# Kernel optimization log

Hardware: AMD Instinct MI355X
Metric: run time of the kernel (lower is better)

## Reference

```python
import jax, jax.numpy as jnp
import numpy as np

N_NODES = 50000
N_EDGES = 800000
FEAT = 128


def setup_inputs() -> dict:
    key = jax.random.key(0)
    k1, k2, k3, k4 = jax.random.split(key, 4)
    x = jax.random.normal(k1, (N_NODES, FEAT), dtype=jnp.float32)
    a = jax.random.normal(k2, (FEAT, 1), dtype=jnp.float32) * (1.414 / np.sqrt(FEAT))
    row = jax.random.randint(k3, (N_EDGES,), 0, N_NODES, dtype=jnp.int64)
    col = jax.random.randint(k4, (N_EDGES,), 0, N_NODES, dtype=jnp.int64)
    return {"x": x, "a": a, "row": row, "col": col}


def reference(x, a, row, col):
    n = x.shape[0]
    # per-node score e = x @ a, squeezed to [N]
    e = jnp.squeeze(x @ a, axis=-1)
    # gather per-edge score from the destination (column) node, as in e[col]
    vals = e[col]                                            # [E]
    # sparse row-wise softmax (numerically stable via segment max)
    m = jax.ops.segment_max(vals, row, num_segments=n)       # [N]
    m = jnp.where(jnp.isfinite(m), m, 0.0)                   # empty rows -> 0
    ex = jnp.exp(vals - m[row])                              # [E]
    denom = jax.ops.segment_sum(ex, row, num_segments=n)     # [N]
    att = ex / denom[row]                                    # [E]
    # sparse-dense matmul: h[i] = sum_j att_ij * x[j]
    h_prime = jax.ops.segment_sum(att[:, None] * x[col], row, num_segments=n)
    return h_prime
```

## Files before the change

kernel.cpp:

```cpp
#include <hip/hip_runtime.h>
#include <hip/hip_bf16.h>
#include <math.h>

#define FEAT 128

__device__ __forceinline__ int pack_bf162(float lo, float hi) {
    __hip_bfloat162 b = __float22bfloat162_rn(make_float2(lo, hi));
    union { __hip_bfloat162 b; int i; } u;
    u.b = b;
    return u.i;
}

__device__ __forceinline__ float2 bf2_to_f2(int b) {
    union { int i; __hip_bfloat162 b; } u;
    u.i = b;
    return __bfloat1622float2(u.b);
}

__global__ void dot_hist_kernel(const float* __restrict__ x, const float* __restrict__ a,
                                const int* __restrict__ row,
                                float* __restrict__ exw, unsigned* __restrict__ cnt,
                                unsigned short* __restrict__ rank,
                                int2* __restrict__ xh, int n, int nE) {
    int tid = blockIdx.x * blockDim.x + threadIdx.x;
    if (tid < nE) {
        unsigned old = atomicAdd(&cnt[row[tid]], 1u);
        rank[tid] = (unsigned short)old;
    }
    int node = tid >> 5;
    int l = tid & 31;
    if (node >= n) return;
    float4 xv = ((const float4*)(x + (size_t)node * FEAT))[l];
    float4 av = ((const float4*)a)[l];
    int2 pk;
    pk.x = pack_bf162(xv.x, xv.y);
    pk.y = pack_bf162(xv.z, xv.w);
    xh[(size_t)node * 32 + l] = pk;
    float p = xv.x * av.x + xv.y * av.y + xv.z * av.z + xv.w * av.w;
    #pragma unroll
    for (int off = 16; off > 0; off >>= 1) p += __shfl_xor(p, off);
    if (l == 0) exw[node] = __expf(p);
}

__global__ void scan_kernel(const unsigned* __restrict__ cnt, int* __restrict__ rowptr,
                            unsigned* flags, int n, int nb) {
    __shared__ int sm[256];
    __shared__ int sprefix;
    int b = blockIdx.x;
    int i0 = (b << 10) + (int)threadIdx.x * 4;
    int v0 = (i0 + 0 < n) ? (int)cnt[i0 + 0] : 0;
    int v1 = (i0 + 1 < n) ? (int)cnt[i0 + 1] : 0;
    int v2 = (i0 + 2 < n) ? (int)cnt[i0 + 2] : 0;
    int v3 = (i0 + 3 < n) ? (int)cnt[i0 + 3] : 0;
    int t4 = v0 + v1 + v2 + v3;
    sm[threadIdx.x] = t4;
    __syncthreads();
    #pragma unroll
    for (int off = 1; off < 256; off <<= 1) {
        int u = (threadIdx.x >= (unsigned)off) ? sm[threadIdx.x - off] : 0;
        __syncthreads();
        sm[threadIdx.x] += u;
        __syncthreads();
    }
    if (threadIdx.x == 0)
        __hip_atomic_store(&flags[b], (unsigned)sm[255] + 1u, __ATOMIC_RELEASE,
                           __HIP_MEMORY_SCOPE_AGENT);
    if (threadIdx.x < 64) {
        int lane = threadIdx.x;
        unsigned pred = 0;
        if (lane < b) {
            unsigned f;
            do {
                f = __hip_atomic_load(&flags[lane], __ATOMIC_ACQUIRE,
                                      __HIP_MEMORY_SCOPE_AGENT);
            } while (f == 0u);
            pred = f - 1u;
        }
        #pragma unroll
        for (int off = 32; off > 0; off >>= 1) pred += __shfl_xor(pred, off);
        if (lane == 0) sprefix = (int)pred;
    }
    __syncthreads();
    int base = sprefix + sm[threadIdx.x] - t4;
    if (i0 + 0 < n) rowptr[i0 + 0] = base;
    if (i0 + 1 < n) rowptr[i0 + 1] = base + v0;
    if (i0 + 2 < n) rowptr[i0 + 2] = base + v0 + v1;
    if (i0 + 3 < n) rowptr[i0 + 3] = base + v0 + v1 + v2;
    if (b == nb - 1 && threadIdx.x == 255) rowptr[n] = sprefix + sm[255];
}

__global__ void fill_kernel(const int* __restrict__ row, const int* __restrict__ col,
                            const unsigned short* __restrict__ rank,
                            const int* __restrict__ rowptr,
                            unsigned short* __restrict__ ecol, int nE) {
    int k = (blockIdx.x * blockDim.x + threadIdx.x) * 4;
    if (k + 3 < nE) {
        int4 r4 = *(const int4*)(row + k);
        int4 c4 = *(const int4*)(col + k);
        uint2 rk = *(const uint2*)(rank + k);
        ecol[rowptr[r4.x] + (int)(rk.x & 0xFFFFu)] = (unsigned short)c4.x;
        ecol[rowptr[r4.y] + (int)(rk.x >> 16)]     = (unsigned short)c4.y;
        ecol[rowptr[r4.z] + (int)(rk.y & 0xFFFFu)] = (unsigned short)c4.z;
        ecol[rowptr[r4.w] + (int)(rk.y >> 16)]     = (unsigned short)c4.w;
    } else {
        for (; k < nE; ++k)
            ecol[rowptr[row[k]] + (int)rank[k]] = (unsigned short)col[k];
    }
}

__global__ void gather_kernel(const int2* __restrict__ xh,
                              const float* __restrict__ exw,
                              const int* __restrict__ rowptr,
                              const unsigned short* __restrict__ ecol,
                              float* __restrict__ h, int n) {
    __shared__ __align__(16) int2 sbuf[8][32];
    int g = threadIdx.x >> 5;
    int lane = threadIdx.x & 31;
    int node = (int)((blockIdx.x * blockDim.x + threadIdx.x) >> 5);
    if (node >= n) return;
    int s = rowptr[node];
    int eend = rowptr[node + 1];
    float4 acc = make_float4(0.f, 0.f, 0.f, 0.f);
    float wsum = 0.0f;
    const int4* sb4 = (const int4*)&sbuf[g][0];
    for (int base = s; base < eend; base += 32) {
        int idx = base + lane;
        float w = 0.0f;
        if (idx < eend) {
            int c = (int)ecol[idx];
            w = exw[c];
            sbuf[g][lane] = make_int2(c << 5, __float_as_int(w));
        }
        #pragma unroll
        for (int off = 16; off > 0; off >>= 1) w += __shfl_xor(w, off);
        wsum += w;
        int m = min(32, eend - base);
        int j = 0;
        for (; j + 4 <= m; j += 4) {
            int4 q0 = sb4[(j >> 1) + 0];
            int4 q1 = sb4[(j >> 1) + 1];
            int2 e0 = xh[q0.x + lane];
            int2 e1 = xh[q0.z + lane];
            int2 e2 = xh[q1.x + lane];
            int2 e3 = xh[q1.z + lane];
            float w0 = __int_as_float(q0.y), w1 = __int_as_float(q0.w);
            float w2 = __int_as_float(q1.y), w3 = __int_as_float(q1.w);
            float2 a0 = bf2_to_f2(e0.x), b0 = bf2_to_f2(e0.y);
            float2 a1 = bf2_to_f2(e1.x), b1 = bf2_to_f2(e1.y);
            float2 a2 = bf2_to_f2(e2.x), b2 = bf2_to_f2(e2.y);
            float2 a3 = bf2_to_f2(e3.x), b3 = bf2_to_f2(e3.y);
            acc.x += w0 * a0.x; acc.y += w0 * a0.y; acc.z += w0 * b0.x; acc.w += w0 * b0.y;
            acc.x += w1 * a1.x; acc.y += w1 * a1.y; acc.z += w1 * b1.x; acc.w += w1 * b1.y;
            acc.x += w2 * a2.x; acc.y += w2 * a2.y; acc.z += w2 * b2.x; acc.w += w2 * b2.y;
            acc.x += w3 * a3.x; acc.y += w3 * a3.y; acc.z += w3 * b3.x; acc.w += w3 * b3.y;
        }
        for (; j < m; ++j) {
            int2 p = sbuf[g][j];
            int2 e = xh[p.x + lane];
            float wj = __int_as_float(p.y);
            float2 aa = bf2_to_f2(e.x), bb = bf2_to_f2(e.y);
            acc.x += wj * aa.x; acc.y += wj * aa.y;
            acc.z += wj * bb.x; acc.w += wj * bb.y;
        }
    }
    float inv = (eend > s) ? 1.0f / wsum : 0.0f;
    float4 out;
    out.x = acc.x * inv;
    out.y = acc.y * inv;
    out.z = acc.z * inv;
    out.w = acc.w * inv;
    ((float4*)(h + (size_t)node * FEAT))[lane] = out;
}

extern "C" void kernel_launch(void* const* d_in, const int* in_sizes, int n_in,
                              void* d_out, int out_size, void* d_ws, size_t ws_size,
                              hipStream_t stream) {
    const float* x = (const float*)d_in[0];
    const float* a = (const float*)d_in[1];
    const int* row = (const int*)d_in[2];
    const int* col = (const int*)d_in[3];
    int n  = in_sizes[0] / FEAT;
    int nE = in_sizes[2];
    float* h = (float*)d_out;
    int nb = (n + 1023) / 1024;

    char* p = (char*)d_ws;
    auto alloc = [&](size_t bytes) { char* q = p; p += (bytes + 15) & ~(size_t)15; return q; };
    unsigned* cnt        = (unsigned*)alloc((size_t)n * 4);
    unsigned* flags      = (unsigned*)alloc(64 * 4);
    float* exw           = (float*)alloc((size_t)n * 4);
    int* rowptr          = (int*)alloc((size_t)(n + 1) * 4);
    unsigned short* rank = (unsigned short*)alloc((size_t)nE * 2);
    unsigned short* ecol = (unsigned short*)alloc((size_t)nE * 2);
    int2* xh             = (int2*)alloc((size_t)n * 32 * 8);

    hipMemsetAsync(cnt, 0, ((size_t)n + 64) * sizeof(unsigned), stream);

    int t1 = (n * 32 > nE) ? n * 32 : nE;
    dot_hist_kernel<<<(t1 + 255) / 256, 256, 0, stream>>>(x, a, row, exw, cnt, rank,
                                                          xh, n, nE);
    scan_kernel<<<nb, 256, 0, stream>>>(cnt, rowptr, flags, n, nb);
    fill_kernel<<<(nE / 4 + 255) / 256, 256, 0, stream>>>(row, col, rank, rowptr,
                                                          ecol, nE);
    gather_kernel<<<(n * 32 + 255) / 256, 256, 0, stream>>>(xh, exw, rowptr, ecol, h, n);
}
```

Baseline: 166.9 us.

## Fuse all stages into one persistent kernel with software grid barriers

Replaces the four separate launches (histogram/dot, scan, fill, gather) with one persistent kernel of 1440 blocks that runs the stages in sequence, separated by atomic-counter grid barriers. The gather stage also changes from 32 lanes with 8-byte loads per node to 16 lanes with 16-byte loads, so each group covers more features per lane. The aim is to remove launch gaps and tail effects between kernels. In exchange it relies on all 1440 blocks being co-resident (launch bounds 6 blocks per CU), with deadlock risk if they are not, and it adds barrier spin cost.

After: 575.2 us. 3.45x slower.

```diff
diff --git a/kernel.cpp b/kernel.cpp
--- a/kernel.cpp
+++ b/kernel.cpp
@@ -3,6 +3,9 @@
 #include <math.h>
 
 #define FEAT 128
+#define GRID 1440
+#define TPB  256
+#define GSZ  (GRID * TPB)
 
 __device__ __forceinline__ int pack_bf162(float lo, float hi) {
     __hip_bfloat162 b = __float22bfloat162_rn(make_float2(lo, hi));
@@ -17,159 +20,186 @@
     return __bfloat1622float2(u.b);
 }
 
-__global__ void dot_hist_kernel(const float* __restrict__ x, const float* __restrict__ a,
-                                const int* __restrict__ row,
-                                float* __restrict__ exw, unsigned* __restrict__ cnt,
-                                unsigned short* __restrict__ rank,
-                                int2* __restrict__ xh, int n, int nE) {
-    int tid = blockIdx.x * blockDim.x + threadIdx.x;
-    if (tid < nE) {
-        unsigned old = atomicAdd(&cnt[row[tid]], 1u);
-        rank[tid] = (unsigned short)old;
-    }
-    int node = tid >> 5;
-    int l = tid & 31;
-    if (node >= n) return;
-    float4 xv = ((const float4*)(x + (size_t)node * FEAT))[l];
-    float4 av = ((const float4*)a)[l];
-    int2 pk;
-    pk.x = pack_bf162(xv.x, xv.y);
-    pk.y = pack_bf162(xv.z, xv.w);
-    xh[(size_t)node * 32 + l] = pk;
-    float p = xv.x * av.x + xv.y * av.y + xv.z * av.z + xv.w * av.w;
-    #pragma unroll
-    for (int off = 16; off > 0; off >>= 1) p += __shfl_xor(p, off);
-    if (l == 0) exw[node] = __expf(p);
-}
-
-__global__ void scan_kernel(const unsigned* __restrict__ cnt, int* __restrict__ rowptr,
-                            unsigned* flags, int n, int nb) {
+__device__ __forceinline__ void fma8(float* acc, int4 v, float w) {
+    float2 f0 = bf2_to_f2(v.x), f1 = bf2_to_f2(v.y);
+    float2 f2 = bf2_to_f2(v.z), f3 = bf2_to_f2(v.w);
+    acc[0] += w * f0.x; acc[1] += w * f0.y;
+    acc[2] += w * f1.x; acc[3] += w * f1.y;
+    acc[4] += w * f2.x; acc[5] += w * f2.y;
+    acc[6] += w * f3.x; acc[7] += w * f3.y;
+}
+
+__device__ __forceinline__ void gridbar(unsigned* bsync, unsigned target) {
+    __syncthreads();
+    if (threadIdx.x == 0) {
+        __hip_atomic_fetch_add(bsync, 1u, __ATOMIC_ACQ_REL, __HIP_MEMORY_SCOPE_AGENT);
+        unsigned v = __hip_atomic_load(bsync, __ATOMIC_ACQUIRE, __HIP_MEMORY_SCOPE_AGENT);
+        while (v < target) {
+            __builtin_amdgcn_s_sleep(2);
+            v = __hip_atomic_load(bsync, __ATOMIC_ACQUIRE, __HIP_MEMORY_SCOPE_AGENT);
+        }
+    }
+    __syncthreads();
+}
+
+extern "C" __global__ void __launch_bounds__(TPB, 6)
+gat_fused(const float* __restrict__ x, const float* __restrict__ a,
+          const int* __restrict__ row, const int* __restrict__ col,
+          float* __restrict__ h,
+          unsigned* __restrict__ cnt, unsigned* __restrict__ flags,
+          unsigned* __restrict__ bsync,
+          float* __restrict__ exw, int* __restrict__ rowptr,
+          unsigned short* __restrict__ rank, unsigned short* __restrict__ ecol,
+          int2* __restrict__ xh, int n, int nE, int nb)
+{
     __shared__ int sm[256];
     __shared__ int sprefix;
-    int b = blockIdx.x;
-    int i0 = (b << 10) + (int)threadIdx.x * 4;
-    int v0 = (i0 + 0 < n) ? (int)cnt[i0 + 0] : 0;
-    int v1 = (i0 + 1 < n) ? (int)cnt[i0 + 1] : 0;
-    int v2 = (i0 + 2 < n) ? (int)cnt[i0 + 2] : 0;
-    int v3 = (i0 + 3 < n) ? (int)cnt[i0 + 3] : 0;
-    int t4 = v0 + v1 + v2 + v3;
-    sm[threadIdx.x] = t4;
-    __syncthreads();
-    #pragma unroll
-    for (int off = 1; off < 256; off <<= 1) {
-        int u = (threadIdx.x >= (unsigned)off) ? sm[threadIdx.x - off] : 0;
-        __syncthreads();
-        sm[threadIdx.x] += u;
-        __syncthreads();
-    }
-    if (threadIdx.x == 0)
-        __hip_atomic_store(&flags[b], (unsigned)sm[255] + 1u, __ATOMIC_RELEASE,
-                           __HIP_MEMORY_SCOPE_AGENT);
-    if (threadIdx.x < 64) {
-        int lane = threadIdx.x;
-        unsigned pred = 0;
-        if (lane < b) {
-            unsigned f;
-            do {
-                f = __hip_atomic_load(&flags[lane], __ATOMIC_ACQUIRE,
-                                      __HIP_MEMORY_SCOPE_AGENT);
-            } while (f == 0u);
-            pred = f - 1u;
-        }
-        #pragma unroll
-        for (int off = 32; off > 0; off >>= 1) pred += __shfl_xor(pred, off);
-        if (lane == 0) sprefix = (int)pred;
-    }
-    __syncthreads();
-    int base = sprefix + sm[threadIdx.x] - t4;
-    if (i0 + 0 < n) rowptr[i0 + 0] = base;
-    if (i0 + 1 < n) rowptr[i0 + 1] = base + v0;
-    if (i0 + 2 < n) rowptr[i0 + 2] = base + v0 + v1;
-    if (i0 + 3 < n) rowptr[i0 + 3] = base + v0 + v1 + v2;
-    if (b == nb - 1 && threadIdx.x == 255) rowptr[n] = sprefix + sm[255];
-}
-
-__global__ void fill_kernel(const int* __restrict__ row, const int* __restrict__ col,
-                            const unsigned short* __restrict__ rank,
-                            const int* __restrict__ rowptr,
-                            unsigned short* __restrict__ ecol, int nE) {
-    int k = (blockIdx.x * blockDim.x + threadIdx.x) * 4;
-    if (k + 3 < nE) {
-        int4 r4 = *(const int4*)(row + k);
-        int4 c4 = *(const int4*)(col + k);
-        uint2 rk = *(const uint2*)(rank + k);
-        ecol[rowptr[r4.x] + (int)(rk.x & 0xFFFFu)] = (unsigned short)c4.x;
-        ecol[rowptr[r4.y] + (int)(rk.x >> 16)]     = (unsigned short)c4.y;
-        ecol[rowptr[r4.z] + (int)(rk.y & 0xFFFFu)] = (unsigned short)c4.z;
-        ecol[rowptr[r4.w] + (int)(rk.y >> 16)]     = (unsigned short)c4.w;
-    } else {
-        for (; k < nE; ++k)
-            ecol[rowptr[row[k]] + (int)rank[k]] = (unsigned short)col[k];
-    }
-}
-
-__global__ void gather_kernel(const int2* __restrict__ xh,
-                              const float* __restrict__ exw,
-                              const int* __restrict__ rowptr,
-                              const unsigned short* __restrict__ ecol,
-                              float* __restrict__ h, int n) {
-    __shared__ __align__(16) int2 sbuf[8][32];
-    int g = threadIdx.x >> 5;
-    int lane = threadIdx.x & 31;
-    int node = (int)((blockIdx.x * blockDim.x + threadIdx.x) >> 5);
-    if (node >= n) return;
-    int s = rowptr[node];
-    int eend = rowptr[node + 1];
-    float4 acc = make_float4(0.f, 0.f, 0.f, 0.f);
-    float wsum = 0.0f;
-    const int4* sb4 = (const int4*)&sbuf[g][0];
-    for (int base = s; base < eend; base += 32) {
-        int idx = base + lane;
-        float w = 0.0f;
-        if (idx < eend) {
-            int c = (int)ecol[idx];
-            w = exw[c];
-            sbuf[g][lane] = make_int2(c << 5, __float_as_int(w));
-        }
-        #pragma unroll
-        for (int off = 16; off > 0; off >>= 1) w += __shfl_xor(w, off);
-        wsum += w;
-        int m = min(32, eend - base);
-        int j = 0;
-        for (; j + 4 <= m; j += 4) {
-            int4 q0 = sb4[(j >> 1) + 0];
-            int4 q1 = sb4[(j >> 1) + 1];
-            int2 e0 = xh[q0.x + lane];
-            int2 e1 = xh[q0.z + lane];
-            int2 e2 = xh[q1.x + lane];
-            int2 e3 = xh[q1.z + lane];
-            float w0 = __int_as_float(q0.y), w1 = __int_as_float(q0.w);
-            float w2 = __int_as_float(q1.y), w3 = __int_as_float(q1.w);
-            float2 a0 = bf2_to_f2(e0.x), b0 = bf2_to_f2(e0.y);
-            float2 a1 = bf2_to_f2(e1.x), b1 = bf2_to_f2(e1.y);
-            float2 a2 = bf2_to_f2(e2.x), b2 = bf2_to_f2(e2.y);
-            float2 a3 = bf2_to_f2(e3.x), b3 = bf2_to_f2(e3.y);
-            acc.x += w0 * a0.x; acc.y += w0 * a0.y; acc.z += w0 * b0.x; acc.w += w0 * b0.y;
-            acc.x += w1 * a1.x; acc.y += w1 * a1.y; acc.z += w1 * b1.x; acc.w += w1 * b1.y;
-            acc.x += w2 * a2.x; acc.y += w2 * a2.y; acc.z += w2 * b2.x; acc.w += w2 * b2.y;
-            acc.x += w3 * a3.x; acc.y += w3 * a3.y; acc.z += w3 * b3.x; acc.w += w3 * b3.y;
-        }
-        for (; j < m; ++j) {
-            int2 p = sbuf[g][j];
-            int2 e = xh[p.x + lane];
-            float wj = __int_as_float(p.y);
-            float2 aa = bf2_to_f2(e.x), bb = bf2_to_f2(e.y);
-            acc.x += wj * aa.x; acc.y += wj * aa.y;
-            acc.z += wj * bb.x; acc.w += wj * bb.y;
-        }
-    }
-    float inv = (eend > s) ? 1.0f / wsum : 0.0f;
-    float4 out;
-    out.x = acc.x * inv;
-    out.y = acc.y * inv;
-    out.z = acc.z * inv;
-    out.w = acc.w * inv;
-    ((float4*)(h + (size_t)node * FEAT))[lane] = out;
+    __shared__ __align__(16) int2 sbuf[16][16];
+
+    const int gid0 = blockIdx.x * TPB + threadIdx.x;
+
+    {
+        int t1 = (n * 32 > nE) ? n * 32 : nE;
+        for (int tid = gid0; tid < t1; tid += GSZ) {
+            if (tid < nE) {
+                unsigned old = atomicAdd(&cnt[row[tid]], 1u);
+                rank[tid] = (unsigned short)old;
+            }
+            int node = tid >> 5;
+            if (node < n) {
+                int l = tid & 31;
+                float4 xv = ((const float4*)(x + (size_t)node * FEAT))[l];
+                float4 av = ((const float4*)a)[l];
+                int2 pk;
+                pk.x = pack_bf162(xv.x, xv.y);
+                pk.y = pack_bf162(xv.z, xv.w);
+                xh[(size_t)node * 32 + l] = pk;
+                float p = xv.x * av.x + xv.y * av.y + xv.z * av.z + xv.w * av.w;
+                #pragma unroll
+                for (int off = 16; off > 0; off >>= 1) p += __shfl_xor(p, off);
+                if (l == 0) exw[node] = __expf(p);
+            }
+        }
+    }
+    gridbar(bsync, GRID);
+
+    {
+        int b = blockIdx.x;
+        if (b < nb) {
+            int i0 = (b << 10) + (int)threadIdx.x * 4;
+            int v0 = (i0 + 0 < n) ? (int)cnt[i0 + 0] : 0;
+            int v1 = (i0 + 1 < n) ? (int)cnt[i0 + 1] : 0;
+            int v2 = (i0 + 2 < n) ? (int)cnt[i0 + 2] : 0;
+            int v3 = (i0 + 3 < n) ? (int)cnt[i0 + 3] : 0;
+            int t4 = v0 + v1 + v2 + v3;
+            sm[threadIdx.x] = t4;
+            __syncthreads();
+            #pragma unroll
+            for (int off = 1; off < 256; off <<= 1) {
+                int u = (threadIdx.x >= (unsigned)off) ? sm[threadIdx.x - off] : 0;
+                __syncthreads();
+                sm[threadIdx.x] += u;
+                __syncthreads();
+            }
+            if (threadIdx.x == 0)
+                __hip_atomic_store(&flags[b], (unsigned)sm[255] + 1u, __ATOMIC_RELEASE,
+                                   __HIP_MEMORY_SCOPE_AGENT);
+            if (threadIdx.x < 64) {
+                int lane = threadIdx.x;
+                unsigned pred = 0;
+                if (lane < b) {
+                    unsigned f;
+                    do {
+                        f = __hip_atomic_load(&flags[lane], __ATOMIC_ACQUIRE,
+                                              __HIP_MEMORY_SCOPE_AGENT);
+                    } while (f == 0u);
+                    pred = f - 1u;
+                }
+                #pragma unroll
+                for (int off = 32; off > 0; off >>= 1) pred += __shfl_xor(pred, off);
+                if (lane == 0) sprefix = (int)pred;
+            }
+            __syncthreads();
+            int base = sprefix + sm[threadIdx.x] - t4;
+            if (i0 + 0 < n) rowptr[i0 + 0] = base;
+            if (i0 + 1 < n) rowptr[i0 + 1] = base + v0;
+            if (i0 + 2 < n) rowptr[i0 + 2] = base + v0 + v1;
+            if (i0 + 3 < n) rowptr[i0 + 3] = base + v0 + v1 + v2;
+            if (b == nb - 1 && threadIdx.x == 255) rowptr[n] = sprefix + sm[255];
+        }
+    }
+    gridbar(bsync, 2u * GRID);
+
+    {
+        int nq = (nE + 3) >> 2;
+        for (int kk = gid0; kk < nq; kk += GSZ) {
+            int k = kk << 2;
+            if (k + 3 < nE) {
+                int4 r4 = *(const int4*)(row + k);
+                int4 c4 = *(const int4*)(col + k);
+                uint2 rk = *(const uint2*)(rank + k);
+                ecol[rowptr[r4.x] + (int)(rk.x & 0xFFFFu)] = (unsigned short)c4.x;
+                ecol[rowptr[r4.y] + (int)(rk.x >> 16)]     = (unsigned short)c4.y;
+                ecol[rowptr[r4.z] + (int)(rk.y & 0xFFFFu)] = (unsigned short)c4.z;
+                ecol[rowptr[r4.w] + (int)(rk.y >> 16)]     = (unsigned short)c4.w;
+            } else {
+                for (; k < nE; ++k)
+                    ecol[rowptr[row[k]] + (int)rank[k]] = (unsigned short)col[k];
+            }
+        }
+    }
+    gridbar(bsync, 3u * GRID);
+
+    {
+        const int4* xh4 = (const int4*)xh;
+        int g = threadIdx.x >> 4;
+        int l = threadIdx.x & 15;
+        int tmax = n * 16;
+        for (int tid = gid0; tid < tmax; tid += GSZ) {
+            int node = tid >> 4;
+            int s0 = rowptr[node];
+            int eend = rowptr[node + 1];
+            float acc[8] = {0.f, 0.f, 0.f, 0.f, 0.f, 0.f, 0.f, 0.f};
+            float wsum = 0.0f;
+            const int4* sb4 = (const int4*)&sbuf[g][0];
+            for (int base = s0; base < eend; base += 16) {
+                int idx = base + l;
+                float w = 0.0f;
+                if (idx < eend) {
+                    int c = (int)ecol[idx];
+                    w = exw[c];
+                    sbuf[g][l] = make_int2(c << 4, __float_as_int(w));
+                }
+                #pragma unroll
+                for (int off = 8; off > 0; off >>= 1) w += __shfl_xor(w, off);
+                wsum += w;
+                int m = min(16, eend - base);
+                int j = 0;
+                for (; j + 4 <= m; j += 4) {
+                    int4 q0 = sb4[(j >> 1) + 0];
+                    int4 q1 = sb4[(j >> 1) + 1];
+                    int4 e0 = xh4[q0.x + l];
+                    int4 e1 = xh4[q0.z + l];
+                    int4 e2 = xh4[q1.x + l];
+                    int4 e3 = xh4[q1.z + l];
+                    fma8(acc, e0, __int_as_float(q0.y));
+                    fma8(acc, e1, __int_as_float(q0.w));
+                    fma8(acc, e2, __int_as_float(q1.y));
+                    fma8(acc, e3, __int_as_float(q1.w));
+                }
+                for (; j < m; ++j) {
+                    int2 p = sbuf[g][j];
+                    fma8(acc, xh4[p.x + l], __int_as_float(p.y));
+                }
+            }
+            float inv = (eend > s0) ? 1.0f / wsum : 0.0f;
+            float4 o0 = make_float4(acc[0] * inv, acc[1] * inv, acc[2] * inv, acc[3] * inv);
+            float4 o1 = make_float4(acc[4] * inv, acc[5] * inv, acc[6] * inv, acc[7] * inv);
+            float4* hp = (float4*)(h + (size_t)node * FEAT);
+            hp[2 * l + 0] = o0;
+            hp[2 * l + 1] = o1;
+        }
+    }
 }
 
 extern "C" void kernel_launch(void* const* d_in, const int* in_sizes, int n_in,
@@ -188,19 +218,15 @@
     auto alloc = [&](size_t bytes) { char* q = p; p += (bytes + 15) & ~(size_t)15; return q; };
     unsigned* cnt        = (unsigned*)alloc((size_t)n * 4);
     unsigned* flags      = (unsigned*)alloc(64 * 4);
+    unsigned* bsync      = (unsigned*)alloc(16 * 4);
     float* exw           = (float*)alloc((size_t)n * 4);
     int* rowptr          = (int*)alloc((size_t)(n + 1) * 4);
     unsigned short* rank = (unsigned short*)alloc((size_t)nE * 2);
     unsigned short* ecol = (unsigned short*)alloc((size_t)nE * 2);
     int2* xh             = (int2*)alloc((size_t)n * 32 * 8);
 
-    hipMemsetAsync(cnt, 0, ((size_t)n + 64) * sizeof(unsigned), stream);
-
-    int t1 = (n * 32 > nE) ? n * 32 : nE;
-    dot_hist_kernel<<<(t1 + 255) / 256, 256, 0, stream>>>(x, a, row, exw, cnt, rank,
-                                                          xh, n, nE);
-    scan_kernel<<<nb, 256, 0, stream>>>(cnt, rowptr, flags, n, nb);
-    fill_kernel<<<(nE / 4 + 255) / 256, 256, 0, stream>>>(row, col, rank, rowptr,
-                                                          ecol, nE);
-    gather_kernel<<<(n * 32 + 255) / 256, 256, 0, stream>>>(xh, exw, rowptr, ecol, h, n);
-}
+    hipMemsetAsync(cnt, 0, (size_t)n * 4 + 64 * 4 + 16 * 4, stream);
+
+    gat_fused<<<GRID, TPB, 0, stream>>>(x, a, row, col, h, cnt, flags, bsync,
+                                        exw, rowptr, rank, ecol, xh, n, nE, nb);
+}
```
